# Performance work log

Measured on AMD Instinct MI355X. Metric: run time of the kernel, lower is better.

The kernel has to match this reference:

```python
import jax, jax.numpy as jnp
import numpy as np

N_NODES = 50000
N_EDGES = 640000
IN_F, H1, H2, H3, N_CLS = 128, 128, 128, 128, 40


def setup_inputs() -> dict:
    key = jax.random.key(0)
    ks = jax.random.split(key, 16)
    def lin(k, i, o):
        bound = 1.0 / np.sqrt(i)
        kw, kb = jax.random.split(k)
        W = jax.random.uniform(kw, (i, o), jnp.float32, -bound, bound)
        b = jax.random.uniform(kb, (o,), jnp.float32, -bound, bound)
        return W, b
    Wr, br = lin(ks[0], IN_F, H3)
    W1, b1 = lin(ks[1], IN_F, H1)
    W2, b2 = lin(ks[2], H1, H2)
    W3, b3 = lin(ks[3], H2, H3)
    Wop, bop = lin(ks[4], H3, N_CLS)
    x = jax.random.normal(ks[5], (N_NODES, IN_F), jnp.float32)
    src = jax.random.randint(ks[6], (N_EDGES,), 0, N_NODES, jnp.int64)
    dst = jax.random.randint(ks[7], (N_EDGES,), 0, N_NODES, jnp.int64)
    edge_weight = jax.random.uniform(ks[8], (N_EDGES,), jnp.float32)
    return {"x": x, "src": src, "dst": dst, "edge_weight": edge_weight,
            "Wr": Wr, "br": br, "W1": W1, "b1": b1, "W2": W2, "b2": b2,
            "W3": W3, "b3": b3, "Wop": Wop, "bop": bop}


def _gconv(x, src, dst, ew, W, b, n_nodes):
    # gather neighbor features, scale by edge weight, scatter-sum to dst, linear
    msg = x[src] * ew[:, None]                      # [E, d_in]
    agg = jax.ops.segment_sum(msg, dst, num_segments=n_nodes)  # [N, d_in]
    return agg @ W + b


def reference(x, src, dst, edge_weight, Wr, br, W1, b1, W2, b2, W3, b3, Wop, bop):
    n = x.shape[0]
    res = x @ Wr + br
    h = jax.nn.relu(_gconv(x, src, dst, edge_weight, W1, b1, n))
    h = jax.nn.relu(_gconv(h, src, dst, edge_weight, W2, b2, n))
    h = _gconv(h, src, dst, edge_weight, W3, b3, n)
    h = jax.nn.relu(h + res)
    return h @ Wop + bop
```

## Files before the change

kernel.cpp:

```cpp
#include <hip/hip_runtime.h>
#include <hip/hip_fp16.h>
#include <stdint.h>


#define NF 128

typedef unsigned short u16;
typedef unsigned int u32;
typedef __attribute__((ext_vector_type(8))) short short8;
typedef __attribute__((ext_vector_type(4))) float f32x4;

__device__ __forceinline__ float bf2f(u16 v) {
    union { unsigned u; float f; } x; x.u = (unsigned)v << 16; return x.f;
}
__device__ __forceinline__ u16 f2bf(float f) {
    union { float f; unsigned u; } x; x.f = f;
    unsigned r = (x.u + 0x7FFFu + ((x.u >> 16) & 1u)) >> 16;
    return (u16)r;
}

__global__ __launch_bounds__(256) void prep_all(
    const int* __restrict__ dst, int* __restrict__ counts, int* __restrict__ rank,
    int n_edges,
    const float* __restrict__ x, u16* __restrict__ xb, int n_feat,
    const float* __restrict__ Wr, const float* __restrict__ W1,
    const float* __restrict__ W2, const float* __restrict__ W3,
    const float* __restrict__ Wop, u16* __restrict__ Wt, u16* __restrict__ Wtop,
    int HB, int CB)
{
    int b = blockIdx.x;
    if (b < HB) {
        int e = b * 256 + threadIdx.x;
        if (e < n_edges) rank[e] = atomicAdd(&counts[dst[e]], 1);
    } else if (b < HB + CB) {
        int idx = ((b - HB) * 256 + threadIdx.x) * 4;
        if (idx < n_feat) {
            float4 v = *reinterpret_cast<const float4*>(x + idx);
            ushort4 o;
            o.x = f2bf(v.x); o.y = f2bf(v.y); o.z = f2bf(v.z); o.w = f2bf(v.w);
            *reinterpret_cast<ushort4*>(xb + idx) = o;
        }
    } else {
        int i = (b - HB - CB) * 256 + threadIdx.x;
        if (i < 4 * 16384) {
            int w = i >> 14, r = i & 16383;
            int nn = r >> 7, kk = r & 127;
            const float* W = (w == 0) ? Wr : (w == 1) ? W1 : (w == 2) ? W2 : W3;
            Wt[i] = f2bf(W[kk * NF + nn]);
        } else {
            int r = i - 4 * 16384;
            if (r < 48 * 128) {
                int nn = r >> 7, kk = r & 127;
                Wtop[r] = (nn < 40) ? f2bf(Wop[kk * 40 + nn]) : (u16)0;
            }
        }
    }
}

__global__ __launch_bounds__(256) void scan_pass1(
    const int* __restrict__ counts, int* __restrict__ bsums, int n)
{
    __shared__ int s[256];
    int i = blockIdx.x * 256 + threadIdx.x;
    int c = (i < n) ? counts[i] : 0;
    s[threadIdx.x] = (c + 3) & ~3;
    __syncthreads();
    for (int off = 128; off > 0; off >>= 1) {
        if (threadIdx.x < off) s[threadIdx.x] += s[threadIdx.x + off];
        __syncthreads();
    }
    if (threadIdx.x == 0) bsums[blockIdx.x] = s[0];
}

__global__ __launch_bounds__(256) void scan_pass23(
    int* __restrict__ rowptr, const int* __restrict__ bsums, int n, int G)
{
    __shared__ int s[256];
    int t = threadIdx.x;
    int bv = (t < G) ? bsums[t] : 0;
    s[t] = bv;
    __syncthreads();
    for (int off = 1; off < 256; off <<= 1) {
        int u = (t >= off) ? s[t - off] : 0;
        __syncthreads();
        s[t] += u;
        __syncthreads();
    }
    int blockoff = (blockIdx.x > 0) ? s[blockIdx.x - 1] : 0;
    int total = s[255];
    __syncthreads();

    int i = blockIdx.x * 256 + t;
    int c = (i < n) ? rowptr[i] : 0;
    int v = (c + 3) & ~3;
    s[t] = v;
    __syncthreads();
    for (int off = 1; off < 256; off <<= 1) {
        int u = (t >= off) ? s[t - off] : 0;
        __syncthreads();
        s[t] += u;
        __syncthreads();
    }
    int excl = s[t] - v + blockoff;
    if (i < n) rowptr[i] = excl;
    if (i == 0) rowptr[n] = total;
}

__global__ __launch_bounds__(256) void fill_packed(
    const int* __restrict__ src, const int* __restrict__ dst,
    const float* __restrict__ ew, const int* __restrict__ rowptr,
    const int* __restrict__ rank, u32* __restrict__ ppairs, int n_edges)
{
    int e = blockIdx.x * 256 + threadIdx.x;
    if (e >= n_edges) return;
    int pos = rowptr[dst[e]] + rank[e];
    ppairs[pos] = ((u32)src[e] << 16) |
                  (u32)__half_as_ushort(__float2half_rn(ew[e]));
}

template<int RES, int PROJ>
__global__ __launch_bounds__(256) void layer_gg(
    const u16* __restrict__ X, const int* __restrict__ rowptr,
    const u32* __restrict__ ppairs, const u16* __restrict__ Wt,
    const float* __restrict__ bias, const u16* __restrict__ resid,
    const u16* __restrict__ Wtop, const float* __restrict__ bop,
    u16* __restrict__ hout, float* __restrict__ out, int n_nodes)
{
    __shared__ u16 As[16 * 128];
    __shared__ u16 Hs[16 * 128];

    const int tid = threadIdx.x;
    const int node0 = blockIdx.x * 16;

    {
        const int nl = tid >> 4;
        const int fl = tid & 15;
        const int node = node0 + nl;
        float acc[8];
        #pragma unroll
        for (int j = 0; j < 8; j++) acc[j] = 0.f;

        if (node < n_nodes) {
            const u16* xf = X + fl * 8;
            int e0 = rowptr[node];
            int e1 = rowptr[node + 1];
            int e = e0;
            for (; e + 8 <= e1; e += 8) {
                uint4 pa = *reinterpret_cast<const uint4*>(ppairs + e);
                uint4 pb = *reinterpret_cast<const uint4*>(ppairs + e + 4);
                u32 p[8] = {pa.x, pa.y, pa.z, pa.w, pb.x, pb.y, pb.z, pb.w};
                short8 v[8];
                #pragma unroll
                for (int k = 0; k < 8; k++)
                    v[k] = *reinterpret_cast<const short8*>(xf + (size_t)(p[k] >> 16) * NF);
                #pragma unroll
                for (int k = 0; k < 8; k++) {
                    float w = __half2float(__ushort_as_half((u16)(p[k] & 0xFFFFu)));
                    #pragma unroll
                    for (int j = 0; j < 8; j++)
                        acc[j] = fmaf(bf2f((u16)v[k][j]), w, acc[j]);
                }
            }
            if (e < e1) {
                uint4 pa = *reinterpret_cast<const uint4*>(ppairs + e);
                u32 p[4] = {pa.x, pa.y, pa.z, pa.w};
                short8 v[4];
                #pragma unroll
                for (int k = 0; k < 4; k++)
                    v[k] = *reinterpret_cast<const short8*>(xf + (size_t)(p[k] >> 16) * NF);
                #pragma unroll
                for (int k = 0; k < 4; k++) {
                    float w = __half2float(__ushort_as_half((u16)(p[k] & 0xFFFFu)));
                    #pragma unroll
                    for (int j = 0; j < 8; j++)
                        acc[j] = fmaf(bf2f((u16)v[k][j]), w, acc[j]);
                }
            }
        }
        short8 o;
        #pragma unroll
        for (int j = 0; j < 8; j++) o[j] = (short)f2bf(acc[j]);
        int gs = fl ^ (nl & 7);
        *reinterpret_cast<short8*>(&As[nl * NF + gs * 8]) = o;
    }
    __syncthreads();

    const int wave = tid >> 6, lane = tid & 63;
    const int lrow = lane & 15, lk = lane >> 4;

    short8 a[4];
    #pragma unroll
    for (int t = 0; t < 4; t++) {
        int g = t * 4 + lk, gs = g ^ (lrow & 7);
        a[t] = *reinterpret_cast<const short8*>(&As[lrow * NF + gs * 8]);
    }

    f32x4 acc2[2];
    #pragma unroll
    for (int ct = 0; ct < 2; ct++) { acc2[ct][0]=0.f; acc2[ct][1]=0.f; acc2[ct][2]=0.f; acc2[ct][3]=0.f; }

    #pragma unroll
    for (int t = 0; t < 4; t++) {
        #pragma unroll
        for (int ct = 0; ct < 2; ct++) {
            int col = wave * 32 + ct * 16 + lrow;
            short8 b = *reinterpret_cast<const short8*>(Wt + (size_t)col * NF + (t * 4 + lk) * 8);
            acc2[ct] = __builtin_amdgcn_mfma_f32_16x16x32_bf16(a[t], b, acc2[ct], 0, 0, 0);
        }
    }

    #pragma unroll
    for (int ct = 0; ct < 2; ct++) {
        int col = wave * 32 + ct * 16 + lrow;
        float bv = bias[col];
        #pragma unroll
        for (int r = 0; r < 4; r++) {
            int row = lk * 4 + r;
            int node = node0 + row;
            if (node < n_nodes) {
                float v = acc2[ct][r] + bv;
                if (RES) v += bf2f(resid[(size_t)node * NF + col]);
                v = fmaxf(v, 0.f);
                if (!PROJ) {
                    hout[(size_t)node * NF + col] = f2bf(v);
                } else {
                    Hs[row * NF + (((col >> 3) ^ (row & 7)) << 3) + (col & 7)] = f2bf(v);
                }
            }
        }
    }

    if (PROJ) {
        __syncthreads();
        if (wave < 3) {
            short8 pa[4];
            #pragma unroll
            for (int t = 0; t < 4; t++) {
                int g = t * 4 + lk, gs = g ^ (lrow & 7);
                pa[t] = *reinterpret_cast<const short8*>(&Hs[lrow * NF + gs * 8]);
            }
            f32x4 pacc;
            pacc[0]=0.f; pacc[1]=0.f; pacc[2]=0.f; pacc[3]=0.f;
            int col = wave * 16 + lrow;
            #pragma unroll
            for (int t = 0; t < 4; t++) {
                short8 b = *reinterpret_cast<const short8*>(Wtop + (size_t)col * NF + (t * 4 + lk) * 8);
                pacc = __builtin_amdgcn_mfma_f32_16x16x32_bf16(pa[t], b, pacc, 0, 0, 0);
            }
            if (col < 40) {
                float bv = bop[col];
                #pragma unroll
                for (int r = 0; r < 4; r++) {
                    int node = node0 + lk * 4 + r;
                    if (node < n_nodes)
                        out[(size_t)node * 40 + col] = pacc[r] + bv;
                }
            }
        }
    }
}

__global__ __launch_bounds__(256) void gemm_mfma_res(
    const u16* __restrict__ A, const u16* __restrict__ Wt,
    const float* __restrict__ bias, u16* __restrict__ out, int nrows)
{
    __shared__ u16 Bs[128 * 128];
    const int tid = threadIdx.x;
    #pragma unroll
    for (int i = 0; i < 8; i++) {
        int G = tid + i * 256;
        int row = G >> 4, g = G & 15, gs = g ^ (row & 7);
        *reinterpret_cast<short8*>(&Bs[row * NF + gs * 8]) =
            *reinterpret_cast<const short8*>(Wt + (size_t)G * 8);
    }

    const int wave = tid >> 6, lane = tid & 63;
    const int lrow = lane & 15, lk = lane >> 4;
    const int row0 = blockIdx.x * 64 + wave * 16;
    const int grow = row0 + lrow;

    short8 a[4];
    if (grow < nrows) {
        const u16* Ar = A + (size_t)grow * NF + lk * 8;
        #pragma unroll
        for (int t = 0; t < 4; t++)
            a[t] = *reinterpret_cast<const short8*>(Ar + t * 32);
    } else {
        #pragma unroll
        for (int t = 0; t < 4; t++)
            #pragma unroll
            for (int j = 0; j < 8; j++) a[t][j] = 0;
    }
    __syncthreads();

    f32x4 acc[8];
    #pragma unroll
    for (int c = 0; c < 8; c++) { acc[c][0]=0.f; acc[c][1]=0.f; acc[c][2]=0.f; acc[c][3]=0.f; }

    #pragma unroll
    for (int t = 0; t < 4; t++) {
        #pragma unroll
        for (int c = 0; c < 8; c++) {
            int col = c * 16 + lrow;
            int g = t * 4 + lk, gs = g ^ (col & 7);
            short8 b = *reinterpret_cast<const short8*>(&Bs[col * NF + gs * 8]);
            acc[c] = __builtin_amdgcn_mfma_f32_16x16x32_bf16(a[t], b, acc[c], 0, 0, 0);
        }
    }

    #pragma unroll
    for (int c = 0; c < 8; c++) {
        int col = c * 16 + lrow;
        float bv = bias[col];
        #pragma unroll
        for (int r = 0; r < 4; r++) {
            int orow = row0 + lk * 4 + r;
            if (orow < nrows)
                out[(size_t)orow * NF + col] = f2bf(acc[c][r] + bv);
        }
    }
}


extern "C" void kernel_launch(void* const* d_in, const int* in_sizes, int n_in,
                              void* d_out, int out_size, void* d_ws, size_t ws_size,
                              hipStream_t stream)
{
    const float* x   = (const float*)d_in[0];
    const int*   src = (const int*)d_in[1];
    const int*   dst = (const int*)d_in[2];
    const float* ew  = (const float*)d_in[3];
    const float* Wr  = (const float*)d_in[4];
    const float* br  = (const float*)d_in[5];
    const float* W1  = (const float*)d_in[6];
    const float* b1  = (const float*)d_in[7];
    const float* W2  = (const float*)d_in[8];
    const float* b2  = (const float*)d_in[9];
    const float* W3  = (const float*)d_in[10];
    const float* b3  = (const float*)d_in[11];
    const float* Wop = (const float*)d_in[12];
    const float* bop = (const float*)d_in[13];
    float* out = (float*)d_out;

    const int n_nodes = in_sizes[0] / NF;
    const int n_edges = in_sizes[1];
    const size_t feat = (size_t)n_nodes * NF;
    const int padded_cap = n_edges + 3 * n_nodes + 8;

    u16* xb   = (u16*)d_ws;
    u16* h1b  = xb + feat;
    u16* h2b  = h1b + feat;
    u16* resb = h2b + feat;
    u16* Wt   = resb + feat;
    u16* Wtop = Wt + 4 * 16384;
    int* rowptr = (int*)(Wtop + 48 * 128);
    const int G1 = (n_nodes + 255) / 256;
    int* bsums  = rowptr + (n_nodes + 1);
    int* rank   = bsums + (G1 + 1);
    u32* ppairs = (u32*)(((uintptr_t)(rank + n_edges) + 15) & ~(uintptr_t)15);

    const int HB = (n_edges + 255) / 256;
    const int CB = ((int)feat / 4 + 255) / 256;
    const int PB = (4 * 16384 + 48 * 128 + 255) / 256;
    const int res_grid   = (n_nodes + 63) / 64;
    const int layer_grid = (n_nodes + 15) / 16;

    hipMemsetAsync(rowptr, 0, (size_t)(n_nodes + 1) * sizeof(int), stream);
    hipMemsetAsync(ppairs, 0, (size_t)padded_cap * sizeof(u32), stream);
    prep_all<<<HB + CB + PB, 256, 0, stream>>>(
        dst, rowptr, rank, n_edges, x, xb, (int)feat,
        Wr, W1, W2, W3, Wop, Wt, Wtop, HB, CB);
    scan_pass1<<<G1, 256, 0, stream>>>(rowptr, bsums, n_nodes);
    scan_pass23<<<G1, 256, 0, stream>>>(rowptr, bsums, n_nodes, G1);
    fill_packed<<<HB, 256, 0, stream>>>(src, dst, ew, rowptr, rank, ppairs, n_edges);

    gemm_mfma_res<<<res_grid, 256, 0, stream>>>(xb, Wt, br, resb, n_nodes);

    layer_gg<0, 0><<<layer_grid, 256, 0, stream>>>(
        xb, rowptr, ppairs, Wt + 16384, b1, nullptr, nullptr, nullptr,
        h1b, nullptr, n_nodes);
    layer_gg<0, 0><<<layer_grid, 256, 0, stream>>>(
        h1b, rowptr, ppairs, Wt + 2 * 16384, b2, nullptr, nullptr, nullptr,
        h2b, nullptr, n_nodes);
    layer_gg<1, 1><<<layer_grid, 256, 0, stream>>>(
        h2b, rowptr, ppairs, Wt + 3 * 16384, b3, resb, Wtop, bop,
        nullptr, out, n_nodes);
}
```

Before: 191.1 us.

## Sort nodes by padded degree bucket to balance per-block gather work

Builds a degree histogram during the row-pointer scan, scans it, and scatters node ids into a permutation grouped by degree bucket. The three graph layers then process nodes in that order, so each 16-node block holds nodes of similar degree and the wavefronts diverge less in the edge loop. The cost is two extra small kernels, an O(256) per-thread rank loop in deg_place, and scattered output writes because the rows of a block are no longer contiguous nodes.

New measurement: 493.6 us. +158.3%, slower.

```diff
diff --git a/kernel.cpp b/kernel.cpp
--- a/kernel.cpp
+++ b/kernel.cpp
@@ -73,7 +73,8 @@
 }
 
 __global__ __launch_bounds__(256) void scan_pass23(
-    int* __restrict__ rowptr, const int* __restrict__ bsums, int n, int G)
+    int* __restrict__ rowptr, const int* __restrict__ bsums,
+    int* __restrict__ ghist, int n, int G)
 {
     __shared__ int s[256];
     int t = threadIdx.x;
@@ -102,8 +103,56 @@
         __syncthreads();
     }
     int excl = s[t] - v + blockoff;
-    if (i < n) rowptr[i] = excl;
+    if (i < n) {
+        rowptr[i] = excl;
+        atomicAdd(&ghist[min(v >> 2, 63)], 1);
+    }
     if (i == 0) rowptr[n] = total;
+}
+
+__global__ __launch_bounds__(64) void deg_scan(
+    const int* __restrict__ ghist, int* __restrict__ gcur)
+{
+    __shared__ int s[64];
+    int t = threadIdx.x;
+    int h = ghist[t];
+    s[t] = h;
+    __syncthreads();
+    for (int off = 1; off < 64; off <<= 1) {
+        int u = (t + off < 64) ? s[t + off] : 0;
+        __syncthreads();
+        s[t] += u;
+        __syncthreads();
+    }
+    gcur[t] = s[t] - h;
+}
+
+__global__ __launch_bounds__(256) void deg_place(
+    const int* __restrict__ rowptr, int* __restrict__ gcur,
+    int* __restrict__ perm, int n)
+{
+    __shared__ int sbin[256];
+    __shared__ int shist[64];
+    __shared__ int sbase[64];
+    const int t = threadIdx.x;
+    const int i = blockIdx.x * 256 + t;
+    if (t < 64) shist[t] = 0;
+    __syncthreads();
+    int bin = -1;
+    if (i < n) {
+        int deg = rowptr[i + 1] - rowptr[i];
+        bin = min(deg >> 2, 63);
+        atomicAdd(&shist[bin], 1);
+    }
+    sbin[t] = bin;
+    __syncthreads();
+    if (t < 64 && shist[t] > 0) sbase[t] = atomicAdd(&gcur[t], shist[t]);
+    __syncthreads();
+    if (bin >= 0) {
+        int r = 0;
+        for (int u = 0; u < t; ++u) r += (sbin[u] == bin);
+        perm[sbase[bin] + r] = i;
+    }
 }
 
 __global__ __launch_bounds__(256) void fill_packed(
@@ -121,13 +170,15 @@
 template<int RES, int PROJ>
 __global__ __launch_bounds__(256) void layer_gg(
     const u16* __restrict__ X, const int* __restrict__ rowptr,
-    const u32* __restrict__ ppairs, const u16* __restrict__ Wt,
+    const u32* __restrict__ ppairs, const int* __restrict__ perm,
+    const u16* __restrict__ Wt,
     const float* __restrict__ bias, const u16* __restrict__ resid,
     const u16* __restrict__ Wtop, const float* __restrict__ bop,
     u16* __restrict__ hout, float* __restrict__ out, int n_nodes)
 {
     __shared__ u16 As[16 * 128];
     __shared__ u16 Hs[16 * 128];
+    __shared__ int pnodes[16];
 
     const int tid = threadIdx.x;
     const int node0 = blockIdx.x * 16;
@@ -135,12 +186,14 @@
     {
         const int nl = tid >> 4;
         const int fl = tid & 15;
-        const int node = node0 + nl;
+        const int idx = node0 + nl;
+        const int node = (idx < n_nodes) ? perm[idx] : -1;
+        if (fl == 0) pnodes[nl] = node;
         float acc[8];
         #pragma unroll
         for (int j = 0; j < 8; j++) acc[j] = 0.f;
 
-        if (node < n_nodes) {
+        if (node >= 0) {
             const u16* xf = X + fl * 8;
             int e0 = rowptr[node];
             int e1 = rowptr[node + 1];
@@ -216,8 +269,8 @@
         #pragma unroll
         for (int r = 0; r < 4; r++) {
             int row = lk * 4 + r;
-            int node = node0 + row;
-            if (node < n_nodes) {
+            int node = pnodes[row];
+            if (node >= 0) {
                 float v = acc2[ct][r] + bv;
                 if (RES) v += bf2f(resid[(size_t)node * NF + col]);
                 v = fmaxf(v, 0.f);
@@ -251,8 +304,8 @@
                 float bv = bop[col];
                 #pragma unroll
                 for (int r = 0; r < 4; r++) {
-                    int node = node0 + lk * 4 + r;
-                    if (node < n_nodes)
+                    int node = pnodes[lk * 4 + r];
+                    if (node >= 0)
                         out[(size_t)node * 40 + col] = pacc[r] + bv;
                 }
             }
@@ -354,10 +407,13 @@
     u16* Wt   = resb + feat;
     u16* Wtop = Wt + 4 * 16384;
     int* rowptr = (int*)(Wtop + 48 * 128);
+    int* ghist  = rowptr + (n_nodes + 1);
+    int* gcur   = ghist + 64;
     const int G1 = (n_nodes + 255) / 256;
-    int* bsums  = rowptr + (n_nodes + 1);
+    int* bsums  = gcur + 64;
     int* rank   = bsums + (G1 + 1);
-    u32* ppairs = (u32*)(((uintptr_t)(rank + n_edges) + 15) & ~(uintptr_t)15);
+    int* perm   = rank + n_edges;
+    u32* ppairs = (u32*)(((uintptr_t)(perm + n_nodes) + 15) & ~(uintptr_t)15);
 
     const int HB = (n_edges + 255) / 256;
     const int CB = ((int)feat / 4 + 255) / 256;
@@ -365,24 +421,26 @@
     const int res_grid   = (n_nodes + 63) / 64;
     const int layer_grid = (n_nodes + 15) / 16;
 
-    hipMemsetAsync(rowptr, 0, (size_t)(n_nodes + 1) * sizeof(int), stream);
+    hipMemsetAsync(rowptr, 0, (size_t)(n_nodes + 1 + 128) * sizeof(int), stream);
     hipMemsetAsync(ppairs, 0, (size_t)padded_cap * sizeof(u32), stream);
     prep_all<<<HB + CB + PB, 256, 0, stream>>>(
         dst, rowptr, rank, n_edges, x, xb, (int)feat,
         Wr, W1, W2, W3, Wop, Wt, Wtop, HB, CB);
     scan_pass1<<<G1, 256, 0, stream>>>(rowptr, bsums, n_nodes);
-    scan_pass23<<<G1, 256, 0, stream>>>(rowptr, bsums, n_nodes, G1);
+    scan_pass23<<<G1, 256, 0, stream>>>(rowptr, bsums, ghist, n_nodes, G1);
+    deg_scan<<<1, 64, 0, stream>>>(ghist, gcur);
+    deg_place<<<G1, 256, 0, stream>>>(rowptr, gcur, perm, n_nodes);
     fill_packed<<<HB, 256, 0, stream>>>(src, dst, ew, rowptr, rank, ppairs, n_edges);
 
     gemm_mfma_res<<<res_grid, 256, 0, stream>>>(xb, Wt, br, resb, n_nodes);
 
     layer_gg<0, 0><<<layer_grid, 256, 0, stream>>>(
-        xb, rowptr, ppairs, Wt + 16384, b1, nullptr, nullptr, nullptr,
+        xb, rowptr, ppairs, perm, Wt + 16384, b1, nullptr, nullptr, nullptr,
         h1b, nullptr, n_nodes);
     layer_gg<0, 0><<<layer_grid, 256, 0, stream>>>(
-        h1b, rowptr, ppairs, Wt + 2 * 16384, b2, nullptr, nullptr, nullptr,
+        h1b, rowptr, ppairs, perm, Wt + 2 * 16384, b2, nullptr, nullptr, nullptr,
         h2b, nullptr, n_nodes);
     layer_gg<1, 1><<<layer_grid, 256, 0, stream>>>(
-        h2b, rowptr, ppairs, Wt + 3 * 16384, b3, resb, Wtop, bop,
+        h2b, rowptr, ppairs, perm, Wt + 3 * 16384, b3, resb, Wtop, bop,
         nullptr, out, n_nodes);
 }
```
